# Optimization experiments

Measured on AMD Instinct MI355X. Metric: run time of the kernel, lower is better.

Reference implementation:

```python
import jax, jax.numpy as jnp
import numpy as np

N_NODES = 50000
N_EDGES = 400000
D_NODE = 256
D_EDGE = 64
LN_EPS = 1e-6  # flax LayerNorm default


def _layer_norm(x, scale, bias):
    mu = jnp.mean(x, axis=-1, keepdims=True)
    var = jnp.mean(jnp.square(x - mu), axis=-1, keepdims=True)
    return (x - mu) * jax.lax.rsqrt(var + LN_EPS) * scale + bias


def _glorot(key, shape):
    fan_in, fan_out = shape
    std = jnp.sqrt(2.0 / (fan_in + fan_out))
    return std * jax.random.normal(key, shape, dtype=jnp.float32)


def setup_inputs() -> dict:
    key = jax.random.key(0)
    ks = jax.random.split(key, 10)
    inp = {
        "nodes": jax.random.normal(ks[0], (N_NODES, D_NODE), dtype=jnp.float32),
        "edges": jax.random.normal(ks[1], (N_EDGES, D_EDGE), dtype=jnp.float32),
        "senders": jax.random.randint(ks[2], (N_EDGES,), 0, N_NODES, dtype=jnp.int32),
        "receivers": jax.random.randint(ks[3], (N_EDGES,), 0, N_NODES, dtype=jnp.int32),
        # message projection (no bias)
        "W_message": _glorot(ks[4], (D_NODE + D_EDGE, D_NODE)),
        # NodeMLP (ReluMLP_skip) with n_features_list_nodes = [256, 256, 256]
        "mlp_W0": _glorot(ks[5], (D_NODE, D_NODE)), "mlp_b0": jnp.zeros((D_NODE,), jnp.float32),
        "mlp_W1": _glorot(ks[6], (D_NODE, D_NODE)), "mlp_b1": jnp.zeros((D_NODE,), jnp.float32),
        "mlp_W2": _glorot(ks[7], (D_NODE, D_NODE)), "mlp_b2": jnp.zeros((D_NODE,), jnp.float32),
        # LayerNorm params
        "ln_aggr_scale": jnp.ones((D_NODE,), jnp.float32), "ln_aggr_bias": jnp.zeros((D_NODE,), jnp.float32),
        "ln_out_scale": jnp.ones((D_NODE,), jnp.float32), "ln_out_bias": jnp.zeros((D_NODE,), jnp.float32),
    }
    return inp


def _relu_mlp_skip(x, Ws, bs):
    # Dense layers; ReLU on all but the last; residual add whenever widths match.
    n = len(Ws)
    for i, (W, b) in enumerate(zip(Ws, bs)):
        y = x @ W + b
        if i < n - 1:
            y = jax.nn.relu(y)
        x = x + y if y.shape[-1] == x.shape[-1] else y
    return x


def reference(nodes, edges, senders, receivers, W_message,
              mlp_W0, mlp_b0, mlp_W1, mlp_b1, mlp_W2, mlp_b2,
              ln_aggr_scale, ln_aggr_bias, ln_out_scale, ln_out_bias):
    total_nodes = nodes.shape[0]
    sender_features = nodes[senders]                      # [E, d] gather
    msg_in = jnp.concatenate([sender_features, edges], axis=-1)  # [E, d+d_e]
    messages = msg_in @ W_message                          # [E, d]
    agg = jax.ops.segment_sum(messages, receivers, num_segments=total_nodes)  # [N, d]
    h = _layer_norm(jax.nn.relu(agg) + nodes, ln_aggr_scale, ln_aggr_bias)
    nodes_out = _relu_mlp_skip(h, [mlp_W0, mlp_W1, mlp_W2], [mlp_b0, mlp_b1, mlp_b2])
    nodes_new = _layer_norm(nodes + nodes_out, ln_out_scale, ln_out_bias)
    return nodes_new
```

## Files before the change

kernel.cpp:

```cpp
#include <hip/hip_runtime.h>

#define NN 50000
#define NE 400000

typedef unsigned short u16;
typedef unsigned int   u32;
typedef __bf16 bf16x4 __attribute__((ext_vector_type(4)));
typedef __bf16 bf16x8 __attribute__((ext_vector_type(8)));
typedef float  f32x16 __attribute__((ext_vector_type(16)));

union ABFrag { bf16x8 v; bf16x4 h[2]; };
union BFrag  { uint4 u; bf16x8 v; };

__device__ __forceinline__ u16 f2bfu(float f) {
  u32 u = __builtin_bit_cast(u32, f);
  return (u16)((u + 0x7FFFu + ((u >> 16) & 1u)) >> 16);
}
__device__ __forceinline__ float bf2f(u16 u) {
  return __builtin_bit_cast(float, (u32)u << 16);
}

__device__ __forceinline__ void pack_one(const float* __restrict__ W,
                                         u16* __restrict__ P, int idx) {
  int k = idx >> 8, n = idx & 255;
  int t16 = k >> 4, kp = k & 15;
  int hh = (kp >> 2) & 1;
  int j = (kp & 3) | (((kp >> 3) & 1) << 2);
  P[(((t16 << 8) + n) << 4) + (hh << 3) + j] = f2bfu(W[idx]);
}

#define NB_CVT  12500
#define NB_PACK 1088
#define NB_HIST 1563

__global__ __launch_bounds__(256) void k_prep(
    const float* __restrict__ nodes, u16* __restrict__ nodes_bf,
    const float* __restrict__ Wm, const float* __restrict__ W0,
    const float* __restrict__ W1, const float* __restrict__ W2,
    u16* __restrict__ Pm, u16* __restrict__ P0,
    u16* __restrict__ P1, u16* __restrict__ P2,
    const int* __restrict__ recv, int* __restrict__ cnt)
{
  int b = blockIdx.x, t = threadIdx.x;
  if (b < NB_CVT) {
    int i = b * 256 + t;
    float4 f = ((const float4*)nodes)[i];
    ushort4 o;
    o.x = f2bfu(f.x); o.y = f2bfu(f.y); o.z = f2bfu(f.z); o.w = f2bfu(f.w);
    ((ushort4*)nodes_bf)[i] = o;
  } else if (b < NB_CVT + NB_PACK) {
    int idx = (b - NB_CVT) * 256 + t;
    const int S0 = 320 * 256, S1 = S0 + 65536, S2 = S1 + 65536;
    if (idx < S0)      pack_one(Wm, Pm, idx);
    else if (idx < S1) pack_one(W0, P0, idx - S0);
    else if (idx < S2) pack_one(W1, P1, idx - S1);
    else               pack_one(W2, P2, idx - S2);
  } else {
    int i = (b - NB_CVT - NB_PACK) * 256 + t;
    if (i < NE) atomicAdd(&cnt[recv[i]], 1);
  }
}

__global__ __launch_bounds__(256) void k_scan1(const int* __restrict__ cnt,
                                               int* __restrict__ loc,
                                               int* __restrict__ bsum) {
  __shared__ int sm[256];
  int t = threadIdx.x, i = blockIdx.x * 256 + t;
  int v = (i < NN) ? cnt[i] : 0;
  sm[t] = v;
  __syncthreads();
  #pragma unroll
  for (int d = 1; d < 256; d <<= 1) {
    int x = sm[t];
    int y = (t >= d) ? sm[t - d] : 0;
    __syncthreads();
    sm[t] = x + y;
    __syncthreads();
  }
  if (i < NN) loc[i] = sm[t] - v;
  if (t == 255) bsum[blockIdx.x] = sm[255];
}

__global__ __launch_bounds__(256) void k_scan2(int* __restrict__ bsum,
                                               int* __restrict__ bpre, int nb) {
  __shared__ int sm[256];
  int t = threadIdx.x;
  int v = (t < nb) ? bsum[t] : 0;
  sm[t] = v;
  __syncthreads();
  #pragma unroll
  for (int d = 1; d < 256; d <<= 1) {
    int x = sm[t];
    int y = (t >= d) ? sm[t - d] : 0;
    __syncthreads();
    sm[t] = x + y;
    __syncthreads();
  }
  if (t < nb) bpre[t] = sm[t] - v;
}

__global__ __launch_bounds__(256) void k_scan3(const int* __restrict__ loc,
                                               const int* __restrict__ bpre,
                                               int* __restrict__ offs,
                                               int* __restrict__ cursor) {
  int i = blockIdx.x * 256 + threadIdx.x;
  if (i < NN) {
    int o = loc[i] + bpre[blockIdx.x];
    offs[i] = o;
    cursor[i] = o;
  }
  if (i == NN - 1) offs[NN] = NE;
}

__global__ __launch_bounds__(256) void k_scatter(
    const int* __restrict__ snd, const int* __restrict__ recv,
    int* __restrict__ cursor, int2* __restrict__ s_pair) {
  int e = blockIdx.x * 256 + threadIdx.x;
  if (e < NE) {
    int p = atomicAdd(&cursor[recv[e]], 1);
    int2 pr; pr.x = snd[e]; pr.y = e;
    s_pair[p] = pr;
  }
}

__global__ __launch_bounds__(256) void k_aggr(
    const u16* __restrict__ nodes_bf, const float* __restrict__ edges,
    const int* __restrict__ offs, const int2* __restrict__ s_pair,
    u16* __restrict__ X)
{
  const int node = blockIdx.x * 4 + (threadIdx.x >> 6);
  const int lane = threadIdx.x & 63;
  const int h = lane >> 5, c = lane & 31;
  const int beg = offs[node], end = offs[node + 1];

  float a0 = 0.f, a1 = 0.f, a2 = 0.f, a3 = 0.f;
  float a4 = 0.f, a5 = 0.f, a6 = 0.f, a7 = 0.f;
  float ae0 = 0.f, ae1 = 0.f;

  for (int jb = beg; jb < end; jb += 8) {
    int j = jb + (lane & 7);
    if (j >= end) j = end - 1;
    int2 pr = s_pair[j];
    const int rem = end - jb;

#define PGATHER(K) \
    int s##K = __shfl(pr.x, 2 * K + h); \
    int e##K = __shfl(pr.y, 2 * K + h); \
    uint4 n##K = *(const uint4*)(nodes_bf + (size_t)s##K * 256 + (c << 3)); \
    float2 v##K = *(const float2*)(edges + (size_t)e##K * 64 + (c << 1));

    PGATHER(0) PGATHER(1) PGATHER(2) PGATHER(3)
#undef PGATHER

#define PACC(K) \
    if (rem > 2 * K + h) { \
      a0 += bf2f((u16)n##K.x); a1 += bf2f((u16)(n##K.x >> 16)); \
      a2 += bf2f((u16)n##K.y); a3 += bf2f((u16)(n##K.y >> 16)); \
      a4 += bf2f((u16)n##K.z); a5 += bf2f((u16)(n##K.z >> 16)); \
      a6 += bf2f((u16)n##K.w); a7 += bf2f((u16)(n##K.w >> 16)); \
      ae0 += v##K.x; ae1 += v##K.y; }

    PACC(0) PACC(1) PACC(2) PACC(3)
#undef PACC
  }

  a0 += __shfl_xor(a0, 32); a1 += __shfl_xor(a1, 32);
  a2 += __shfl_xor(a2, 32); a3 += __shfl_xor(a3, 32);
  a4 += __shfl_xor(a4, 32); a5 += __shfl_xor(a5, 32);
  a6 += __shfl_xor(a6, 32); a7 += __shfl_xor(a7, 32);
  ae0 += __shfl_xor(ae0, 32); ae1 += __shfl_xor(ae1, 32);

  if (lane < 32) {
    u16* xr = X + (size_t)node * 320;
    uint4 o;
    o.x = (u32)f2bfu(a0) | ((u32)f2bfu(a1) << 16);
    o.y = (u32)f2bfu(a2) | ((u32)f2bfu(a3) << 16);
    o.z = (u32)f2bfu(a4) | ((u32)f2bfu(a5) << 16);
    o.w = (u32)f2bfu(a6) | ((u32)f2bfu(a7) << 16);
    *(uint4*)(xr + (c << 3)) = o;
    *(u32*)(xr + 256 + (c << 1)) =
        (u32)f2bfu(ae0) | ((u32)f2bfu(ae1) << 16);
  }
}


#define AT_ADDR(r, c) (atb + ((((r) * 640) + ((c) * 2)) ^ (((r) & 7) << 4)))

#define WRBT32(c, v) do { int _c = (c); \
  *(uint4*)&Bt[((_c >> 9) << 12) + ((_c & 1) << 11) + (((_c >> 1) & 255) << 3)] = (v); \
} while (0)

#define MFMA_STEP32(t) \
  _Pragma("unroll") \
  for (int s = 0; s < 2; ++s) { \
    ABFrag a; \
    const int kc = ((t) << 5) + (s << 4) + (h << 2); \
    a.h[0] = *(const bf16x4*)AT_ADDR(mrow, kc); \
    a.h[1] = *(const bf16x4*)AT_ADDR(mrow, kc + 8); \
    const int bi = (s << 12) + (h << 11) + ((wcn + m32) << 3); \
    BFrag bA, bB; \
    bA.u = *(const uint4*)&Bt[bi]; \
    bB.u = *(const uint4*)&Bt[bi + 256]; \
    accA = __builtin_amdgcn_mfma_f32_32x32x16_bf16(a.v, bA.v, accA, 0, 0, 0); \
    accB = __builtin_amdgcn_mfma_f32_32x32x16_bf16(a.v, bB.v, accB, 0, 0, 0); \
  }

#define RUN_LAYER32(wp, T) do { \
  const u16* pb = (wp) + ((size_t)tid << 3); \
  uint4 p0 = *(const uint4*)(pb); \
  uint4 p1 = *(const uint4*)(pb + 4096); \
  _Pragma("unroll 1") \
  for (int t = 0; t < (T); ++t) { \
    __syncthreads(); \
    WRBT32(tid, p0); WRBT32(tid + 512, p1); \
    if (t + 1 < (T)) { \
      const u16* nb = pb + ((size_t)(t + 1) << 13); \
      p0 = *(const uint4*)nb; p1 = *(const uint4*)(nb + 4096); \
    } \
    __syncthreads(); \
    MFMA_STEP32(t) \
  } \
} while (0)

#define ROW_OF(rg) (((rg) & 3) + (((rg) >> 2) << 3) + (h << 2))

#define LN_STATS32() do { \
  _Pragma("unroll") \
  for (int rg = 0; rg < 16; ++rg) { \
    float va = accA[rg], vb = accB[rg]; \
    float s = va + vb, s2 = va * va + vb * vb; \
    s  += __shfl_xor(s, 1);  s  += __shfl_xor(s, 2);  s  += __shfl_xor(s, 4); \
    s  += __shfl_xor(s, 8);  s  += __shfl_xor(s, 16); \
    s2 += __shfl_xor(s2, 1); s2 += __shfl_xor(s2, 2); s2 += __shfl_xor(s2, 4); \
    s2 += __shfl_xor(s2, 8); s2 += __shfl_xor(s2, 16); \
    if (m32 == 0) { int mm = wr32 + ROW_OF(rg); red[mm][wc2] = s; red[mm][wc2 + 1] = s2; } \
  } \
  __syncthreads(); \
  if (tid < 64) { \
    float s  = red[tid][0] + red[tid][2] + red[tid][4] + red[tid][6]; \
    float s2 = red[tid][1] + red[tid][3] + red[tid][5] + red[tid][7]; \
    float mu  = s * (1.f / 256.f); \
    float var = s2 * (1.f / 256.f) - mu * mu; \
    murs[tid][0] = mu; murs[tid][1] = rsqrtf(var + 1e-6f); \
  } \
  __syncthreads(); \
} while (0)

__global__ __launch_bounds__(512)
void k_fused(
    const u16* __restrict__ X, const float* __restrict__ nodes,
    const u16* __restrict__ wm, const u16* __restrict__ w0,
    const u16* __restrict__ w1, const u16* __restrict__ w2,
    const float* __restrict__ b0, const float* __restrict__ b1,
    const float* __restrict__ b2,
    const float* __restrict__ lnAs, const float* __restrict__ lnAb,
    const float* __restrict__ lnOs, const float* __restrict__ lnOb,
    float* __restrict__ out)
{
  __shared__ u16 At[64 * 320];
  __shared__ u16 Bt[8192];
  __shared__ float red[64][8];
  __shared__ float murs[64][2];

  const int tid = threadIdx.x;
  const int lane = tid & 63;
  const int w = tid >> 6;
  const int wr32 = (w >> 2) << 5;
  const int wcn = (w & 3) << 6;
  const int wc2 = (w & 3) << 1;
  const int m32 = lane & 31, h = lane >> 5;
  const int mrow = wr32 + m32;
  const int r0 = blockIdx.x * 64;

  char* const atb = (char*)At;

  #pragma unroll
  for (int it = 0; it < 5; ++it) {
    int c = tid + it * 512;
    int r = c / 40, seg = c - r * 40;
    int row = r0 + r;
    uint4 v = {0u, 0u, 0u, 0u};
    if (row < NN) v = *(const uint4*)(X + (size_t)row * 320 + seg * 8);
    *(uint4*)(atb + ((r * 640 + seg * 16) ^ ((r & 7) << 4))) = v;
  }

  f32x16 accA, accB;
  #pragma unroll
  for (int i = 0; i < 16; ++i) { accA[i] = 0.f; accB[i] = 0.f; }

  RUN_LAYER32(wm, 10);

  #pragma unroll
  for (int rg = 0; rg < 16; ++rg) {
    int row = r0 + wr32 + ROW_OF(rg);
    float nA = 0.f, nB = 0.f;
    if (row < NN) {
      nA = nodes[(size_t)row * 256 + wcn + m32];
      nB = nodes[(size_t)row * 256 + wcn + 32 + m32];
    }
    accA[rg] = fmaxf(accA[rg], 0.f) + nA;
    accB[rg] = fmaxf(accB[rg], 0.f) + nB;
  }
  LN_STATS32();
  {
    float sclA = lnAs[wcn + m32], biaA = lnAb[wcn + m32];
    float sclB = lnAs[wcn + 32 + m32], biaB = lnAb[wcn + 32 + m32];
    #pragma unroll
    for (int rg = 0; rg < 16; ++rg) {
      int mm = wr32 + ROW_OF(rg);
      float mu = murs[mm][0], rs = murs[mm][1];
      float hA = (accA[rg] - mu) * rs * sclA + biaA;
      float hB = (accB[rg] - mu) * rs * sclB + biaB;
      *(u16*)AT_ADDR(mm, wcn + m32) = f2bfu(hA);
      *(u16*)AT_ADDR(mm, wcn + 32 + m32) = f2bfu(hB);
      accA[rg] = 0.f; accB[rg] = 0.f;
    }
  }

  #pragma unroll 1
  for (int l = 0; l < 3; ++l) {
    const u16* wp = (l == 0) ? w0 : (l == 1) ? w1 : w2;
    RUN_LAYER32(wp, 8);
    __syncthreads();

    if (l < 2) {
      const float* bp = (l == 0) ? b0 : b1;
      float bnA = bp[wcn + m32], bnB = bp[wcn + 32 + m32];
      #pragma unroll
      for (int rg = 0; rg < 16; ++rg) {
        int mm = wr32 + ROW_OF(rg);
        u16* pA = (u16*)AT_ADDR(mm, wcn + m32);
        u16* pB = (u16*)AT_ADDR(mm, wcn + 32 + m32);
        float xA = bf2f(*pA) + fmaxf(accA[rg] + bnA, 0.f);
        float xB = bf2f(*pB) + fmaxf(accB[rg] + bnB, 0.f);
        *pA = f2bfu(xA);
        *pB = f2bfu(xB);
        accA[rg] = 0.f; accB[rg] = 0.f;
      }
    } else {
      float bnA = b2[wcn + m32], bnB = b2[wcn + 32 + m32];
      #pragma unroll
      for (int rg = 0; rg < 16; ++rg) {
        int mm = wr32 + ROW_OF(rg);
        int row = r0 + mm;
        float nA = 0.f, nB = 0.f;
        if (row < NN) {
          nA = nodes[(size_t)row * 256 + wcn + m32];
          nB = nodes[(size_t)row * 256 + wcn + 32 + m32];
        }
        accA[rg] = nA + bf2f(*(const u16*)AT_ADDR(mm, wcn + m32)) + accA[rg] + bnA;
        accB[rg] = nB + bf2f(*(const u16*)AT_ADDR(mm, wcn + 32 + m32)) + accB[rg] + bnB;
      }
    }
  }

  LN_STATS32();
  {
    float sclA = lnOs[wcn + m32], biaA = lnOb[wcn + m32];
    float sclB = lnOs[wcn + 32 + m32], biaB = lnOb[wcn + 32 + m32];
    #pragma unroll
    for (int rg = 0; rg < 16; ++rg) {
      int mm = wr32 + ROW_OF(rg);
      int row = r0 + mm;
      if (row < NN) {
        float mu = murs[mm][0], rs = murs[mm][1];
        out[(size_t)row * 256 + wcn + m32] = (accA[rg] - mu) * rs * sclA + biaA;
        out[(size_t)row * 256 + wcn + 32 + m32] = (accB[rg] - mu) * rs * sclB + biaB;
      }
    }
  }
}

extern "C" void kernel_launch(void* const* d_in, const int* in_sizes, int n_in,
                              void* d_out, int out_size, void* d_ws, size_t ws_size,
                              hipStream_t stream)
{
  const float* nodes = (const float*)d_in[0];
  const float* edges = (const float*)d_in[1];
  const int* senders = (const int*)d_in[2];
  const int* receivers = (const int*)d_in[3];
  const float* Wmsg = (const float*)d_in[4];
  const float* W0 = (const float*)d_in[5];
  const float* b0 = (const float*)d_in[6];
  const float* W1 = (const float*)d_in[7];
  const float* b1 = (const float*)d_in[8];
  const float* W2 = (const float*)d_in[9];
  const float* b2 = (const float*)d_in[10];
  const float* lnAs = (const float*)d_in[11];
  const float* lnAb = (const float*)d_in[12];
  const float* lnOs = (const float*)d_in[13];
  const float* lnOb = (const float*)d_in[14];
  float* out = (float*)d_out;
  (void)in_sizes; (void)n_in; (void)out_size; (void)ws_size;

  char* w = (char*)d_ws;
  size_t off = 0;
  auto take = [&](size_t b) { void* p = w + off; off += (b + 511) & ~(size_t)511; return p; };

  u16*   nodes_bf = (u16*)take((size_t)NN * 256 * 2);
  u16*   wmsg_p   = (u16*)take(320 * 256 * 2);
  u16*   w0_p     = (u16*)take(256 * 256 * 2);
  u16*   w1_p     = (u16*)take(256 * 256 * 2);
  u16*   w2_p     = (u16*)take(256 * 256 * 2);
  u16*   X        = (u16*)take((size_t)NN * 320 * 2);
  int*   cnt      = (int*)take((size_t)NN * 4);
  int*   loc      = (int*)take((size_t)NN * 4);
  int*   offs     = (int*)take((size_t)(NN + 1) * 4);
  int*   cursor   = (int*)take((size_t)NN * 4);
  int2*  s_pair   = (int2*)take((size_t)NE * 8);
  int*   bsum     = (int*)take(256 * 4);
  int*   bpre     = (int*)take(256 * 4);

  const int NB = (NN + 255) / 256;

  hipMemsetAsync(cnt, 0, (size_t)NN * 4, stream);
  k_prep<<<NB_CVT + NB_PACK + NB_HIST, 256, 0, stream>>>(
      nodes, nodes_bf, Wmsg, W0, W1, W2, wmsg_p, w0_p, w1_p, w2_p,
      receivers, cnt);

  k_scan1<<<NB, 256, 0, stream>>>(cnt, loc, bsum);
  k_scan2<<<1, 256, 0, stream>>>(bsum, bpre, NB);
  k_scan3<<<NB, 256, 0, stream>>>(loc, bpre, offs, cursor);
  k_scatter<<<(NE + 255) / 256, 256, 0, stream>>>(senders, receivers, cursor, s_pair);

  k_aggr<<<NN / 4, 256, 0, stream>>>(nodes_bf, edges, offs, s_pair, X);

  const int MB = (NN + 63) / 64;
  k_fused<<<MB, 512, 0, stream>>>(X, nodes, wmsg_p, w0_p, w1_p, w2_p,
                                  b0, b1, b2, lnAs, lnAb, lnOs, lnOb, out);
}
```

Baseline: 245.1 us.

## Use 16 waves per block in fused MLP kernel, one 32x32 tile each

The fused GEMM/LayerNorm kernel now launches 1024 threads per block instead of 512. Each wave owns a single 32x32 output tile instead of two, and B-tile staging is spread across all threads. This halves accumulator registers per wave and doubles waves available to hide latency. In exchange, each A fragment is reused by only one MFMA, the LN reduction uses more partial sums, and every block-wide barrier now waits on twice as many waves.

Result: slower. 295.7 us (+20.6%).

```diff
diff --git a/kernel.cpp b/kernel.cpp
--- a/kernel.cpp
+++ b/kernel.cpp
@@ -186,59 +186,49 @@
 
 #define AT_ADDR(r, c) (atb + ((((r) * 640) + ((c) * 2)) ^ (((r) & 7) << 4)))
 
-#define WRBT32(c, v) do { int _c = (c); \
-  *(uint4*)&Bt[((_c >> 9) << 12) + ((_c & 1) << 11) + (((_c >> 1) & 255) << 3)] = (v); \
-} while (0)
-
 #define MFMA_STEP32(t) \
   _Pragma("unroll") \
   for (int s = 0; s < 2; ++s) { \
     ABFrag a; \
-    const int kc = ((t) << 5) + (s << 4) + (h << 2); \
+    const int kc = ((t) << 5) + (s << 4) + (hA << 2); \
     a.h[0] = *(const bf16x4*)AT_ADDR(mrow, kc); \
     a.h[1] = *(const bf16x4*)AT_ADDR(mrow, kc + 8); \
-    const int bi = (s << 12) + (h << 11) + ((wcn + m32) << 3); \
-    BFrag bA, bB; \
-    bA.u = *(const uint4*)&Bt[bi]; \
-    bB.u = *(const uint4*)&Bt[bi + 256]; \
-    accA = __builtin_amdgcn_mfma_f32_32x32x16_bf16(a.v, bA.v, accA, 0, 0, 0); \
-    accB = __builtin_amdgcn_mfma_f32_32x32x16_bf16(a.v, bB.v, accB, 0, 0, 0); \
+    BFrag b; \
+    b.u = *(const uint4*)&Bt[(s << 12) + (hA << 11) + (ncol << 3)]; \
+    acc = __builtin_amdgcn_mfma_f32_32x32x16_bf16(a.v, b.v, acc, 0, 0, 0); \
   }
 
 #define RUN_LAYER32(wp, T) do { \
-  const u16* pb = (wp) + ((size_t)tid << 3); \
-  uint4 p0 = *(const uint4*)(pb); \
-  uint4 p1 = *(const uint4*)(pb + 4096); \
+  const u16* pb = (wp) + (sB << 12) + (nB << 4) + (hB << 3); \
+  uint4 p0 = *(const uint4*)pb; \
   _Pragma("unroll 1") \
   for (int t = 0; t < (T); ++t) { \
     __syncthreads(); \
-    WRBT32(tid, p0); WRBT32(tid + 512, p1); \
-    if (t + 1 < (T)) { \
-      const u16* nb = pb + ((size_t)(t + 1) << 13); \
-      p0 = *(const uint4*)nb; p1 = *(const uint4*)(nb + 4096); \
-    } \
+    *(uint4*)&Bt[btidx] = p0; \
+    if (t + 1 < (T)) p0 = *(const uint4*)(pb + ((size_t)(t + 1) << 13)); \
     __syncthreads(); \
     MFMA_STEP32(t) \
   } \
 } while (0)
 
-#define ROW_OF(rg) (((rg) & 3) + (((rg) >> 2) << 3) + (h << 2))
+#define ROW_OF(rg) (((rg) & 3) + (((rg) >> 2) << 3) + (hA << 2))
 
 #define LN_STATS32() do { \
   _Pragma("unroll") \
   for (int rg = 0; rg < 16; ++rg) { \
-    float va = accA[rg], vb = accB[rg]; \
-    float s = va + vb, s2 = va * va + vb * vb; \
+    float v = acc[rg]; \
+    float s = v, s2 = v * v; \
     s  += __shfl_xor(s, 1);  s  += __shfl_xor(s, 2);  s  += __shfl_xor(s, 4); \
     s  += __shfl_xor(s, 8);  s  += __shfl_xor(s, 16); \
     s2 += __shfl_xor(s2, 1); s2 += __shfl_xor(s2, 2); s2 += __shfl_xor(s2, 4); \
     s2 += __shfl_xor(s2, 8); s2 += __shfl_xor(s2, 16); \
-    if (m32 == 0) { int mm = wr32 + ROW_OF(rg); red[mm][wc2] = s; red[mm][wc2 + 1] = s2; } \
+    if (m32 == 0) { int mm = wr32 + ROW_OF(rg); red[mm][wcH] = s; red[mm][wcH + 1] = s2; } \
   } \
   __syncthreads(); \
   if (tid < 64) { \
-    float s  = red[tid][0] + red[tid][2] + red[tid][4] + red[tid][6]; \
-    float s2 = red[tid][1] + red[tid][3] + red[tid][5] + red[tid][7]; \
+    float s = 0.f, s2 = 0.f; \
+    _Pragma("unroll") \
+    for (int i = 0; i < 8; ++i) { s += red[tid][2 * i]; s2 += red[tid][2 * i + 1]; } \
     float mu  = s * (1.f / 256.f); \
     float var = s2 * (1.f / 256.f) - mu * mu; \
     murs[tid][0] = mu; murs[tid][1] = rsqrtf(var + 1e-6f); \
@@ -246,7 +236,7 @@
   __syncthreads(); \
 } while (0)
 
-__global__ __launch_bounds__(512)
+__global__ __launch_bounds__(1024)
 void k_fused(
     const u16* __restrict__ X, const float* __restrict__ nodes,
     const u16* __restrict__ wm, const u16* __restrict__ w0,
@@ -259,61 +249,57 @@
 {
   __shared__ u16 At[64 * 320];
   __shared__ u16 Bt[8192];
-  __shared__ float red[64][8];
+  __shared__ float red[64][16];
   __shared__ float murs[64][2];
 
   const int tid = threadIdx.x;
   const int lane = tid & 63;
   const int w = tid >> 6;
-  const int wr32 = (w >> 2) << 5;
-  const int wcn = (w & 3) << 6;
-  const int wc2 = (w & 3) << 1;
-  const int m32 = lane & 31, h = lane >> 5;
+  const int wr32 = (w >> 3) << 5;
+  const int wc = w & 7;
+  const int wcH = wc << 1;
+  const int m32 = lane & 31, hA = lane >> 5;
+  const int ncol = (wc << 5) + m32;
   const int mrow = wr32 + m32;
   const int r0 = blockIdx.x * 64;
+  const int sB = tid >> 9, hB = (tid >> 8) & 1, nB = tid & 255;
+  const int btidx = (sB << 12) + (hB << 11) + (nB << 3);
 
   char* const atb = (char*)At;
 
   #pragma unroll
-  for (int it = 0; it < 5; ++it) {
-    int c = tid + it * 512;
-    int r = c / 40, seg = c - r * 40;
-    int row = r0 + r;
-    uint4 v = {0u, 0u, 0u, 0u};
-    if (row < NN) v = *(const uint4*)(X + (size_t)row * 320 + seg * 8);
-    *(uint4*)(atb + ((r * 640 + seg * 16) ^ ((r & 7) << 4))) = v;
-  }
-
-  f32x16 accA, accB;
+  for (int it = 0; it < 3; ++it) {
+    int c = tid + it * 1024;
+    if (c < 2560) {
+      int r = c / 40, seg = c - r * 40;
+      int row = r0 + r;
+      uint4 v = {0u, 0u, 0u, 0u};
+      if (row < NN) v = *(const uint4*)(X + (size_t)row * 320 + seg * 8);
+      *(uint4*)(atb + ((r * 640 + seg * 16) ^ ((r & 7) << 4))) = v;
+    }
+  }
+
+  f32x16 acc;
   #pragma unroll
-  for (int i = 0; i < 16; ++i) { accA[i] = 0.f; accB[i] = 0.f; }
+  for (int i = 0; i < 16; ++i) acc[i] = 0.f;
 
   RUN_LAYER32(wm, 10);
 
   #pragma unroll
   for (int rg = 0; rg < 16; ++rg) {
     int row = r0 + wr32 + ROW_OF(rg);
-    float nA = 0.f, nB = 0.f;
-    if (row < NN) {
-      nA = nodes[(size_t)row * 256 + wcn + m32];
-      nB = nodes[(size_t)row * 256 + wcn + 32 + m32];
-    }
-    accA[rg] = fmaxf(accA[rg], 0.f) + nA;
-    accB[rg] = fmaxf(accB[rg], 0.f) + nB;
+    float nv = (row < NN) ? nodes[(size_t)row * 256 + ncol] : 0.f;
+    acc[rg] = fmaxf(acc[rg], 0.f) + nv;
   }
   LN_STATS32();
   {
-    float sclA = lnAs[wcn + m32], biaA = lnAb[wcn + m32];
-    float sclB = lnAs[wcn + 32 + m32], biaB = lnAb[wcn + 32 + m32];
+    float scl = lnAs[ncol], bia = lnAb[ncol];
     #pragma unroll
     for (int rg = 0; rg < 16; ++rg) {
       int mm = wr32 + ROW_OF(rg);
-      float mu = murs[mm][0], rs = murs[mm][1];
-      float hA = (accA[rg] - mu) * rs * sclA + biaA;
-      float hB = (accB[rg] - mu) * rs * sclB + biaB;
-      *(u16*)AT_ADDR(mm, wcn + m32) = f2bfu(hA);
-      *(u16*)AT_ADDR(mm, wcn + 32 + m32) = f2bfu(hB);
-      accA[rg] = 0.f; accB[rg] = 0.f;
+      float hv = (acc[rg] - murs[mm][0]) * murs[mm][1] * scl + bia;
+      *(u16*)AT_ADDR(mm, ncol) = f2bfu(hv);
+      acc[rg] = 0.f;
     }
   }
 
@@ -325,48 +311,37 @@
 
     if (l < 2) {
       const float* bp = (l == 0) ? b0 : b1;
-      float bnA = bp[wcn + m32], bnB = bp[wcn + 32 + m32];
+      float bn = bp[ncol];
       #pragma unroll
       for (int rg = 0; rg < 16; ++rg) {
         int mm = wr32 + ROW_OF(rg);
-        u16* pA = (u16*)AT_ADDR(mm, wcn + m32);
-        u16* pB = (u16*)AT_ADDR(mm, wcn + 32 + m32);
-        float xA = bf2f(*pA) + fmaxf(accA[rg] + bnA, 0.f);
-        float xB = bf2f(*pB) + fmaxf(accB[rg] + bnB, 0.f);
-        *pA = f2bfu(xA);
-        *pB = f2bfu(xB);
-        accA[rg] = 0.f; accB[rg] = 0.f;
+        u16* p = (u16*)AT_ADDR(mm, ncol);
+        float xn = bf2f(*p) + fmaxf(acc[rg] + bn, 0.f);
+        *p = f2bfu(xn);
+        acc[rg] = 0.f;
       }
     } else {
-      float bnA = b2[wcn + m32], bnB = b2[wcn + 32 + m32];
+      float bn = b2[ncol];
       #pragma unroll
       for (int rg = 0; rg < 16; ++rg) {
         int mm = wr32 + ROW_OF(rg);
         int row = r0 + mm;
-        float nA = 0.f, nB = 0.f;
-        if (row < NN) {
-          nA = nodes[(size_t)row * 256 + wcn + m32];
-          nB = nodes[(size_t)row * 256 + wcn + 32 + m32];
-        }
-        accA[rg] = nA + bf2f(*(const u16*)AT_ADDR(mm, wcn + m32)) + accA[rg] + bnA;
-        accB[rg] = nB + bf2f(*(const u16*)AT_ADDR(mm, wcn + 32 + m32)) + accB[rg] + bnB;
+        float nv = (row < NN) ? nodes[(size_t)row * 256 + ncol] : 0.f;
+        acc[rg] = nv + bf2f(*(const u16*)AT_ADDR(mm, ncol)) + acc[rg] + bn;
       }
     }
   }
 
   LN_STATS32();
   {
-    float sclA = lnOs[wcn + m32], biaA = lnOb[wcn + m32];
-    float sclB = lnOs[wcn + 32 + m32], biaB = lnOb[wcn + 32 + m32];
+    float scl = lnOs[ncol], bia = lnOb[ncol];
     #pragma unroll
     for (int rg = 0; rg < 16; ++rg) {
       int mm = wr32 + ROW_OF(rg);
       int row = r0 + mm;
-      if (row < NN) {
-        float mu = murs[mm][0], rs = murs[mm][1];
-        out[(size_t)row * 256 + wcn + m32] = (accA[rg] - mu) * rs * sclA + biaA;
-        out[(size_t)row * 256 + wcn + 32 + m32] = (accB[rg] - mu) * rs * sclB + biaB;
-      }
+      if (row < NN)
+        out[(size_t)row * 256 + ncol] =
+            (acc[rg] - murs[mm][0]) * murs[mm][1] * scl + bia;
     }
   }
 }
@@ -426,6 +401,6 @@
   k_aggr<<<NN / 4, 256, 0, stream>>>(nodes_bf, edges, offs, s_pair, X);
 
   const int MB = (NN + 63) / 64;
-  k_fused<<<MB, 512, 0, stream>>>(X, nodes, wmsg_p, w0_p, w1_p, w2_p,
-                                  b0, b1, b2, lnAs, lnAb, lnOs, lnOb, out);
-}
+  k_fused<<<MB, 1024, 0, stream>>>(X, nodes, wmsg_p, w0_p, w1_p, w2_p,
+                                   b0, b1, b2, lnAs, lnAb, lnOs, lnOb, out);
+}
```
